# Kernel optimization log

Hardware: AMD Instinct MI355X
Metric: run time of the kernel (lower is better)

The kernel has to match this reference:

```python
import jax, jax.numpy as jnp
import numpy as np

SR = 48000
SECONDS = 2.0
T = int(SECONDS * SR)  # 96000 samples


def _shift(x, n):
    """Delay 1-D signal x by n samples, zero-filling (n may be a traced int >= 0)."""
    t = jnp.arange(x.shape[0])
    return jnp.where(t >= n, jnp.roll(x, n), jnp.zeros((), x.dtype))


def setup_inputs() -> dict:
    key = jax.random.key(0)
    k1, k2 = jax.random.split(key)
    excitation = jax.random.normal(k1, (T,), dtype=jnp.float32)
    pluckPosition = jax.random.uniform(k2, (1,), dtype=jnp.float32, minval=0.1, maxval=0.9)
    return {
        "length": 240,  # delay-line length in samples -> f0 = SR/length = 200 Hz
        "pluckPosition": pluckPosition,
        "excitation": excitation,
        "nut_gain": jnp.asarray(-0.99, jnp.float32),    # GuitarNuts reflection
        "bridge_gain": jnp.asarray(-0.995, jnp.float32),  # GuitarBridge reflection
        "bridge_b": jnp.asarray(0.5, jnp.float32),      # bridge one-zero lowpass coeff
        "disp_a": jnp.asarray(0.3, jnp.float32),        # dispersion FIR coeff
    }


def reference(length, pluckPosition, excitation, nut_gain, bridge_gain, bridge_b, disp_a):
    L = int(length)
    pluck = pluckPosition[0]
    nUp = jnp.round(L * pluck).astype(jnp.int32)   # StringSegment(nUp)
    nDown = jnp.int32(L) - nUp                      # StringSegment(nDown)

    def bridge_lp(x):
        # one-zero lowpass at the bridge: y[t] = (1-b)*x[t] + b*x[t-1]
        return (1.0 - bridge_b) * x + bridge_b * _shift(x, 1)

    def dispersion(x):
        # two-tap FIR dispersion filter: y[t] = a*x[t] + (1-a)*x[t-1]
        return disp_a * x + (1.0 - disp_a) * _shift(x, 1)

    def vibrate(l, r):
        # right-going wave: up segment -> dispersion -> down segment
        r2 = _shift(dispersion(_shift(r, nUp)), nDown)
        # left-going wave: down segment -> dispersion -> up segment
        l2 = _shift(dispersion(_shift(l, nDown)), nUp)
        return l2, r2

    # _start: inject excitation (split between the two traveling waves at pluck point)
    left0 = _shift(0.5 * excitation, nDown)
    right0 = _shift(0.5 * excitation, nUp)

    n_iter = T // L  # len(excitation) // int(length)

    def step(carry, _):
        l, r, acc = carry
        r_new = nut_gain * l                      # _lterminate: nut reflection of left wave
        l_new = bridge_gain * bridge_lp(r)        # _rterminate: bridge reflection of right wave
        l_new, r_new = vibrate(l_new, r_new)      # _vibrate: propagate through segments
        return (l_new, r_new, acc + l_new + r_new), None

    acc0 = left0 + right0
    (_, _, acc), _ = jax.lax.scan(step, (left0, right0, acc0), None, length=n_iter)
    return acc  # sum(left_signal) + sum(right_signal), shape [T]
```

## Files before the change

### kernel.cpp

```cpp
#include <hip/hip_runtime.h>


#define PREP_BLK 1024
#define SPAN_MAX 4640
#define SEQ_BLK  256

template<int NA, int NB>
static __device__ __forceinline__ void convT(const float* a, const float* b, float* c) {
#pragma unroll
    for (int i = 0; i < NA + NB - 1; ++i) c[i] = 0.f;
#pragma unroll
    for (int i = 0; i < NA; ++i)
#pragma unroll
        for (int j = 0; j < NB; ++j) c[i + j] += a[i] * b[j];
}

struct Base {
    int L, nUp, nDown;
    float gb, gn, g;
    float c0, c1, c2, d0, d1;
    float e[4];
};

static __device__ __forceinline__ Base mkbase(const int* Lp, const float* pk,
        const float* gnp, const float* gbp, const float* bbp, const float* dap) {
    Base b;
    b.L = Lp[0];
    b.gn = gnp[0]; b.gb = gbp[0];
    const float bb = bbp[0], da = dap[0];
    b.nUp   = (int)rintf((float)b.L * pk[0]);
    b.nDown = b.L - b.nUp;
    b.c0 = da * (1.f - bb);
    b.c1 = da * bb + (1.f - da) * (1.f - bb);
    b.c2 = (1.f - da) * bb;
    b.d0 = da; b.d1 = 1.f - da;
    b.e[0] = b.c0*b.d0;
    b.e[1] = b.c0*b.d1 + b.c1*b.d0;
    b.e[2] = b.c1*b.d1 + b.c2*b.d0;
    b.e[3] = b.c2*b.d1;
    b.g = b.gb * b.gn;
    return b;
}

__global__ __launch_bounds__(PREP_BLK, 1)
void prep_kernel(const int* Lp, const float* pk, const float* __restrict__ exc,
                 const float* gnp, const float* gbp, const float* bbp, const float* dap,
                 float* __restrict__ D4l, float* __restrict__ D4r, int T) {
    __shared__ float Dls[SPAN_MAX];
    __shared__ float Drs[SPAN_MAX];

    const Base B = mkbase(Lp, pk, gnp, gbp, bbp, dap);
    float p2[7], p3[10], p4[13], p5[16], p6[19], p7[22];
    convT<4,4>(B.e, B.e, p2);
    convT<7,4>(p2, B.e, p3);
    convT<7,7>(p2, p2, p4);
    convT<13,4>(p4, B.e, p5);
    convT<13,7>(p4, p2, p6);
    convT<13,10>(p4, p3, p7);
    const float g = B.g, g2 = g*g, g3 = g2*g, g4 = g2*g2, g5 = g4*g, g6 = g4*g2, g7 = g4*g3;

    const int P0   = 2 * B.L;
    const int H    = 7 * P0 + 21;
    const int span = PREP_BLK + H;
    const int t0   = blockIdx.x * PREP_BLK;
    const int base = t0 - H;

    const int mx = (B.nUp > B.nDown) ? B.nUp : B.nDown;
    const bool safe = (base - B.L - mx - 2) >= 0;

    for (int j = threadIdx.x; j < span; j += PREP_BLK) {
        const int s = base + j;
        float dl, dr;
        if (safe) {
            dl = 0.5f * exc[s - B.nDown]
               + (0.5f * B.gb) * (B.c0 * exc[s - B.L     - B.nUp]
                                + B.c1 * exc[s - B.L - 1 - B.nUp]
                                + B.c2 * exc[s - B.L - 2 - B.nUp]);
            dr = 0.5f * exc[s - B.nUp]
               + (0.5f * B.gn) * (B.d0 * exc[s - B.L     - B.nDown]
                                + B.d1 * exc[s - B.L - 1 - B.nDown]);
        } else {
            auto ex = [&](int i) -> float { return (i >= 0) ? exc[i] : 0.f; };
            if (s < 0) { dl = 0.f; dr = 0.f; }
            else {
                dl = 0.5f * ex(s - B.nDown)
                   + (0.5f * B.gb) * (B.c0 * ex(s - B.L     - B.nUp)
                                    + B.c1 * ex(s - B.L - 1 - B.nUp)
                                    + B.c2 * ex(s - B.L - 2 - B.nUp));
                dr = 0.5f * ex(s - B.nUp)
                   + (0.5f * B.gn) * (B.d0 * ex(s - B.L     - B.nDown)
                                    + B.d1 * ex(s - B.L - 1 - B.nDown));
            }
        }
        Dls[j] = dl; Drs[j] = dr;
    }
    __syncthreads();

    const int t = t0 + threadIdx.x;
    if (t < T) {
        const int p = H + threadIdx.x;
        float al = Dls[p], ar = Drs[p];
#pragma unroll
        for (int k = 0; k < 4;  ++k) { const int j = p -     P0 - k; const float w = g  * B.e[k]; al += w*Dls[j]; ar += w*Drs[j]; }
#pragma unroll
        for (int k = 0; k < 7;  ++k) { const int j = p - 2 * P0 - k; const float w = g2 * p2[k];  al += w*Dls[j]; ar += w*Drs[j]; }
#pragma unroll
        for (int k = 0; k < 10; ++k) { const int j = p - 3 * P0 - k; const float w = g3 * p3[k];  al += w*Dls[j]; ar += w*Drs[j]; }
#pragma unroll
        for (int k = 0; k < 13; ++k) { const int j = p - 4 * P0 - k; const float w = g4 * p4[k];  al += w*Dls[j]; ar += w*Drs[j]; }
#pragma unroll
        for (int k = 0; k < 16; ++k) { const int j = p - 5 * P0 - k; const float w = g5 * p5[k];  al += w*Dls[j]; ar += w*Drs[j]; }
#pragma unroll
        for (int k = 0; k < 19; ++k) { const int j = p - 6 * P0 - k; const float w = g6 * p6[k];  al += w*Dls[j]; ar += w*Drs[j]; }
#pragma unroll
        for (int k = 0; k < 22; ++k) { const int j = p - 7 * P0 - k; const float w = g7 * p7[k];  al += w*Dls[j]; ar += w*Drs[j]; }
        D4l[t] = al; D4r[t] = ar;
    }
}

__global__ __launch_bounds__(SEQ_BLK, 1)
void seq_kernel(const int* Lp, const float* pk, const float* gnp, const float* gbp,
                const float* bbp, const float* dap,
                float* __restrict__ Slw, float* __restrict__ Srw, int T) {
    __shared__ float4 pl[2][4][256];
    __shared__ float4 pre[4][6];

    const Base B = mkbase(Lp, pk, gnp, gbp, bbp, dap);
    float p2[7], p4[13], f[25];
    convT<4,4>(B.e, B.e, p2);
    convT<7,7>(p2, p2, p4);
    convT<13,13>(p4, p4, f);
    const float g2 = B.g * B.g, g4 = g2 * g2, G = g4 * g4;

    const int L = B.L, P = 16 * L, NA = L;
    const int lam = threadIdx.x;
    const bool act = lam < NA;
    float* __restrict__ DD = blockIdx.x ? Srw : Slw;

    {   float4* z = &pl[0][0][0];
        for (int i = lam; i < 2*4*256; i += SEQ_BLK) z[i] = float4{0,0,0,0};
        if (lam < 24) (&pre[0][0])[lam] = float4{0,0,0,0};
    }
    __syncthreads();

    const int nphase = (T + P - 1) / P;

    auto load16 = [&](int t, float4& a, float4& b, float4& c, float4& d) {
        if (t + 16 <= T) {
            a = *(const float4*)(DD + t);      b = *(const float4*)(DD + t + 4);
            c = *(const float4*)(DD + t + 8); d = *(const float4*)(DD + t + 12);
        } else {
            float tmp[16];
#pragma unroll
            for (int s = 0; s < 16; ++s) tmp[s] = (t + s < T) ? DD[t + s] : 0.f;
            a = float4{tmp[0],tmp[1],tmp[2],tmp[3]};   b = float4{tmp[4],tmp[5],tmp[6],tmp[7]};
            c = float4{tmp[8],tmp[9],tmp[10],tmp[11]}; d = float4{tmp[12],tmp[13],tmp[14],tmp[15]};
        }
    };

    float4 dE[4] = {{0,0,0,0},{0,0,0,0},{0,0,0,0},{0,0,0,0}};
    float4 dO[4] = {{0,0,0,0},{0,0,0,0},{0,0,0,0},{0,0,0,0}};
    if (act)               load16(lam << 4,     dE[0], dE[1], dE[2], dE[3]);
    if (act && nphase > 1) load16(P + (lam<<4), dO[0], dO[1], dO[2], dO[3]);

    float4 pS0{0,0,0,0}, pS1{0,0,0,0}, pS2{0,0,0,0}, pS3{0,0,0,0};

    auto do_phase = [&](int q, float4 (&dv)[4]) {
        const int par = q & 1, pp = par ^ 1, rs = (q + 2) & 3, wsl = q & 3;

        float4 B2{0,0,0,0}, B3{0,0,0,0}, A0{0,0,0,0}, A1{0,0,0,0}, A2{0,0,0,0}, A3{0,0,0,0};
        if (act) {
            if (lam >= 2) {
                B2 = pl[pp][2][lam-2]; B3 = pl[pp][3][lam-2];
                A0 = pl[pp][0][lam-1]; A1 = pl[pp][1][lam-1];
                A2 = pl[pp][2][lam-1]; A3 = pl[pp][3][lam-1];
            } else if (lam == 1) {
                B2 = pre[rs][4]; B3 = pre[rs][5];
                A0 = pl[pp][0][0]; A1 = pl[pp][1][0];
                A2 = pl[pp][2][0]; A3 = pl[pp][3][0];
            } else {
                B2 = pre[rs][0]; B3 = pre[rs][1];
                A0 = pre[rs][2]; A1 = pre[rs][3];
                A2 = pre[rs][4]; A3 = pre[rs][5];
            }
        }

        float S[16];
        if (act) {
            float cw[40];
            cw[0]=B2.x; cw[1]=B2.y; cw[2]=B2.z; cw[3]=B2.w;
            cw[4]=B3.x; cw[5]=B3.y; cw[6]=B3.z; cw[7]=B3.w;
            cw[8]=A0.x; cw[9]=A0.y; cw[10]=A0.z; cw[11]=A0.w;
            cw[12]=A1.x; cw[13]=A1.y; cw[14]=A1.z; cw[15]=A1.w;
            cw[16]=A2.x; cw[17]=A2.y; cw[18]=A2.z; cw[19]=A2.w;
            cw[20]=A3.x; cw[21]=A3.y; cw[22]=A3.z; cw[23]=A3.w;
            cw[24]=pS0.x; cw[25]=pS0.y; cw[26]=pS0.z; cw[27]=pS0.w;
            cw[28]=pS1.x; cw[29]=pS1.y; cw[30]=pS1.z; cw[31]=pS1.w;
            cw[32]=pS2.x; cw[33]=pS2.y; cw[34]=pS2.z; cw[35]=pS2.w;
            cw[36]=pS3.x; cw[37]=pS3.y; cw[38]=pS3.z; cw[39]=pS3.w;
            const float dvf[16] = {dv[0].x,dv[0].y,dv[0].z,dv[0].w,
                                   dv[1].x,dv[1].y,dv[1].z,dv[1].w,
                                   dv[2].x,dv[2].y,dv[2].z,dv[2].w,
                                   dv[3].x,dv[3].y,dv[3].z,dv[3].w};
#pragma unroll
            for (int s = 0; s < 16; ++s) {
                float a0 = 0.f, a1 = 0.f;
#pragma unroll
                for (int k = 0; k < 25; k += 2) a0 += f[k] * cw[24 + s - k];
#pragma unroll
                for (int k = 1; k < 25; k += 2) a1 += f[k] * cw[24 + s - k];
                S[s] = dvf[s] + G * (a0 + a1);
            }
        }

        if (act && (q + 2) < nphase) load16((q + 2) * P + (lam << 4), dv[0], dv[1], dv[2], dv[3]);

        if (act) {
            pS0 = float4{S[0],S[1],S[2],S[3]};   pS1 = float4{S[4],S[5],S[6],S[7]};
            pS2 = float4{S[8],S[9],S[10],S[11]}; pS3 = float4{S[12],S[13],S[14],S[15]};
            pl[par][0][lam] = pS0; pl[par][1][lam] = pS1;
            pl[par][2][lam] = pS2; pl[par][3][lam] = pS3;
            if (lam == NA - 2) { pre[wsl][0] = pS2; pre[wsl][1] = pS3; }
            if (lam == NA - 1) { pre[wsl][2] = pS0; pre[wsl][3] = pS1;
                                 pre[wsl][4] = pS2; pre[wsl][5] = pS3; }
            const int tg = q * P + (lam << 4);
            if (tg + 16 <= T) {
                *(float4*)(DD + tg)      = pS0; *(float4*)(DD + tg + 4)  = pS1;
                *(float4*)(DD + tg + 8)  = pS2; *(float4*)(DD + tg + 12) = pS3;
            } else {
#pragma unroll
                for (int s = 0; s < 16; ++s) if (tg + s < T) DD[tg + s] = S[s];
            }
        }

        asm volatile("s_waitcnt lgkmcnt(0)" ::: "memory");
        __builtin_amdgcn_sched_barrier(0);
        __builtin_amdgcn_s_barrier();
        __builtin_amdgcn_sched_barrier(0);
    };

    int q = 0;
    for (; q + 1 < nphase; q += 2) { do_phase(q, dE); do_phase(q + 1, dO); }
    if (q < nphase) do_phase(q, dE);
}

__global__ void add_kernel(const float* __restrict__ a, const float* __restrict__ b,
                           float* __restrict__ o, int T) {
    const int i = (blockIdx.x * blockDim.x + threadIdx.x) * 4;
    if (i + 4 <= T) {
        const float4 x = *(const float4*)(a + i);
        const float4 y = *(const float4*)(b + i);
        *(float4*)(o + i) = float4{x.x + y.x, x.y + y.y, x.z + y.z, x.w + y.w};
    } else if (i < T) {
        for (int s = i; s < T; ++s) o[s] = a[s] + b[s];
    }
}

extern "C" void kernel_launch(void* const* d_in, const int* in_sizes, int n_in,
                              void* d_out, int out_size, void* d_ws, size_t ws_size,
                              hipStream_t stream) {
    const int*   Lp  = (const int*)  d_in[0];
    const float* pk  = (const float*)d_in[1];
    const float* exc = (const float*)d_in[2];
    const float* gn  = (const float*)d_in[3];
    const float* gb  = (const float*)d_in[4];
    const float* bb  = (const float*)d_in[5];
    const float* da  = (const float*)d_in[6];
    float* out = (float*)d_out;
    float* D4l = (float*)d_ws;
    float* D4r = D4l + out_size;
    const int T = out_size;

    prep_kernel<<<(T + PREP_BLK - 1) / PREP_BLK, PREP_BLK, 0, stream>>>(
        Lp, pk, exc, gn, gb, bb, da, D4l, D4r, T);
    seq_kernel<<<2, SEQ_BLK, 0, stream>>>(Lp, pk, gn, gb, bb, da, D4l, D4r, T);
    add_kernel<<<(T / 4 + 255) / 256, 256, 0, stream>>>(D4l, D4r, out, T);
}
```

Measured before the change: 55.80 us.

## Halve per-thread span in sequential recurrence kernel and add clock warm-up probe

The sequential recurrence kernel now uses 2L threads, each computing 8 samples instead of 16, so per-thread FIR work per phase is halved. The shared-memory halo exchange is reworked to take three neighbour lanes and three carried-over boundary entries. A dummy FMA-spinning kernel is launched before the sequential kernel, apparently to raise GPU clocks. That probe adds launch time and extra work, and the larger block adds barrier cost across more waves.

Measured after the change: 56.18 us. No clear change (+0.7%).

```diff
diff --git a/kernel.cpp b/kernel.cpp
--- a/kernel.cpp
+++ b/kernel.cpp
@@ -3,7 +3,7 @@
 
 #define PREP_BLK 1024
 #define SPAN_MAX 4640
-#define SEQ_BLK  256
+#define SEQ_BLK  512
 
 template<int NA, int NB>
 static __device__ __forceinline__ void convT(const float* a, const float* b, float* c) {
@@ -118,11 +118,30 @@
     }
 }
 
+__global__ __launch_bounds__(256, 4)
+void clock_probe_kernel(int iters) {
+    float a0 = threadIdx.x * 1e-9f + 0.10f, a1 = a0 + 0.01f, a2 = a0 + 0.02f,
+          a3 = a0 + 0.03f, a4 = a0 + 0.04f, a5 = a0 + 0.05f, a6 = a0 + 0.06f,
+          a7 = a0 + 0.07f;
+    for (int i = 0; i < iters; ++i) {
+        a0 = __builtin_fmaf(a0, 0.9999f, 1e-7f);
+        a1 = __builtin_fmaf(a1, 0.9999f, 1e-7f);
+        a2 = __builtin_fmaf(a2, 0.9999f, 1e-7f);
+        a3 = __builtin_fmaf(a3, 0.9999f, 1e-7f);
+        a4 = __builtin_fmaf(a4, 0.9999f, 1e-7f);
+        a5 = __builtin_fmaf(a5, 0.9999f, 1e-7f);
+        a6 = __builtin_fmaf(a6, 0.9999f, 1e-7f);
+        a7 = __builtin_fmaf(a7, 0.9999f, 1e-7f);
+    }
+    asm volatile("" :: "v"(a0), "v"(a1), "v"(a2), "v"(a3),
+                       "v"(a4), "v"(a5), "v"(a6), "v"(a7));
+}
+
 __global__ __launch_bounds__(SEQ_BLK, 1)
 void seq_kernel(const int* Lp, const float* pk, const float* gnp, const float* gbp,
                 const float* bbp, const float* dap,
                 float* __restrict__ Slw, float* __restrict__ Srw, int T) {
-    __shared__ float4 pl[2][4][256];
+    __shared__ float4 pl[2][2][512];
     __shared__ float4 pre[4][6];
 
     const Base B = mkbase(Lp, pk, gnp, gbp, bbp, dap);
@@ -132,78 +151,73 @@
     convT<13,13>(p4, p4, f);
     const float g2 = B.g * B.g, g4 = g2 * g2, G = g4 * g4;
 
-    const int L = B.L, P = 16 * L, NA = L;
+    const int L = B.L, P = 16 * L, NA = 2 * L;
     const int lam = threadIdx.x;
     const bool act = lam < NA;
     float* __restrict__ DD = blockIdx.x ? Srw : Slw;
 
     {   float4* z = &pl[0][0][0];
-        for (int i = lam; i < 2*4*256; i += SEQ_BLK) z[i] = float4{0,0,0,0};
+        for (int i = lam; i < 2*2*512; i += SEQ_BLK) z[i] = float4{0,0,0,0};
         if (lam < 24) (&pre[0][0])[lam] = float4{0,0,0,0};
     }
     __syncthreads();
 
     const int nphase = (T + P - 1) / P;
 
-    auto load16 = [&](int t, float4& a, float4& b, float4& c, float4& d) {
-        if (t + 16 <= T) {
-            a = *(const float4*)(DD + t);      b = *(const float4*)(DD + t + 4);
-            c = *(const float4*)(DD + t + 8); d = *(const float4*)(DD + t + 12);
+    auto load8 = [&](int t, float4& a, float4& b) {
+        if (t + 8 <= T) {
+            a = *(const float4*)(DD + t); b = *(const float4*)(DD + t + 4);
         } else {
-            float tmp[16];
-#pragma unroll
-            for (int s = 0; s < 16; ++s) tmp[s] = (t + s < T) ? DD[t + s] : 0.f;
-            a = float4{tmp[0],tmp[1],tmp[2],tmp[3]};   b = float4{tmp[4],tmp[5],tmp[6],tmp[7]};
-            c = float4{tmp[8],tmp[9],tmp[10],tmp[11]}; d = float4{tmp[12],tmp[13],tmp[14],tmp[15]};
+            float tmp[8];
+#pragma unroll
+            for (int s = 0; s < 8; ++s) tmp[s] = (t + s < T) ? DD[t + s] : 0.f;
+            a = float4{tmp[0],tmp[1],tmp[2],tmp[3]};
+            b = float4{tmp[4],tmp[5],tmp[6],tmp[7]};
         }
     };
 
-    float4 dE[4] = {{0,0,0,0},{0,0,0,0},{0,0,0,0},{0,0,0,0}};
-    float4 dO[4] = {{0,0,0,0},{0,0,0,0},{0,0,0,0},{0,0,0,0}};
-    if (act)               load16(lam << 4,     dE[0], dE[1], dE[2], dE[3]);
-    if (act && nphase > 1) load16(P + (lam<<4), dO[0], dO[1], dO[2], dO[3]);
-
-    float4 pS0{0,0,0,0}, pS1{0,0,0,0}, pS2{0,0,0,0}, pS3{0,0,0,0};
-
-    auto do_phase = [&](int q, float4 (&dv)[4]) {
+    float4 dE[2] = {{0,0,0,0},{0,0,0,0}};
+    float4 dO[2] = {{0,0,0,0},{0,0,0,0}};
+    if (act)               load8(lam << 3,       dE[0], dE[1]);
+    if (act && nphase > 1) load8(P + (lam << 3), dO[0], dO[1]);
+
+    float4 pS0{0,0,0,0}, pS1{0,0,0,0};
+
+    auto do_phase = [&](int q, float4 (&dv)[2]) {
         const int par = q & 1, pp = par ^ 1, rs = (q + 2) & 3, wsl = q & 3;
 
-        float4 B2{0,0,0,0}, B3{0,0,0,0}, A0{0,0,0,0}, A1{0,0,0,0}, A2{0,0,0,0}, A3{0,0,0,0};
+        float4 W0{0,0,0,0}, W1{0,0,0,0}, W2{0,0,0,0},
+               W3{0,0,0,0}, W4{0,0,0,0}, W5{0,0,0,0};
         if (act) {
-            if (lam >= 2) {
-                B2 = pl[pp][2][lam-2]; B3 = pl[pp][3][lam-2];
-                A0 = pl[pp][0][lam-1]; A1 = pl[pp][1][lam-1];
-                A2 = pl[pp][2][lam-1]; A3 = pl[pp][3][lam-1];
+            if (lam >= 3) {
+                W0 = pl[pp][0][lam-3]; W1 = pl[pp][1][lam-3];
+                W2 = pl[pp][0][lam-2]; W3 = pl[pp][1][lam-2];
+                W4 = pl[pp][0][lam-1]; W5 = pl[pp][1][lam-1];
+            } else if (lam == 2) {
+                W0 = pre[rs][4]; W1 = pre[rs][5];
+                W2 = pl[pp][0][0]; W3 = pl[pp][1][0];
+                W4 = pl[pp][0][1]; W5 = pl[pp][1][1];
             } else if (lam == 1) {
-                B2 = pre[rs][4]; B3 = pre[rs][5];
-                A0 = pl[pp][0][0]; A1 = pl[pp][1][0];
-                A2 = pl[pp][2][0]; A3 = pl[pp][3][0];
+                W0 = pre[rs][2]; W1 = pre[rs][3];
+                W2 = pre[rs][4]; W3 = pre[rs][5];
+                W4 = pl[pp][0][0]; W5 = pl[pp][1][0];
             } else {
-                B2 = pre[rs][0]; B3 = pre[rs][1];
-                A0 = pre[rs][2]; A1 = pre[rs][3];
-                A2 = pre[rs][4]; A3 = pre[rs][5];
-            }
-        }
-
-        float S[16];
+                W0 = pre[rs][0]; W1 = pre[rs][1];
+                W2 = pre[rs][2]; W3 = pre[rs][3];
+                W4 = pre[rs][4]; W5 = pre[rs][5];
+            }
+        }
+
+        float S[8];
         if (act) {
-            float cw[40];
-            cw[0]=B2.x; cw[1]=B2.y; cw[2]=B2.z; cw[3]=B2.w;
-            cw[4]=B3.x; cw[5]=B3.y; cw[6]=B3.z; cw[7]=B3.w;
-            cw[8]=A0.x; cw[9]=A0.y; cw[10]=A0.z; cw[11]=A0.w;
-            cw[12]=A1.x; cw[13]=A1.y; cw[14]=A1.z; cw[15]=A1.w;
-            cw[16]=A2.x; cw[17]=A2.y; cw[18]=A2.z; cw[19]=A2.w;
-            cw[20]=A3.x; cw[21]=A3.y; cw[22]=A3.z; cw[23]=A3.w;
-            cw[24]=pS0.x; cw[25]=pS0.y; cw[26]=pS0.z; cw[27]=pS0.w;
-            cw[28]=pS1.x; cw[29]=pS1.y; cw[30]=pS1.z; cw[31]=pS1.w;
-            cw[32]=pS2.x; cw[33]=pS2.y; cw[34]=pS2.z; cw[35]=pS2.w;
-            cw[36]=pS3.x; cw[37]=pS3.y; cw[38]=pS3.z; cw[39]=pS3.w;
-            const float dvf[16] = {dv[0].x,dv[0].y,dv[0].z,dv[0].w,
-                                   dv[1].x,dv[1].y,dv[1].z,dv[1].w,
-                                   dv[2].x,dv[2].y,dv[2].z,dv[2].w,
-                                   dv[3].x,dv[3].y,dv[3].z,dv[3].w};
-#pragma unroll
-            for (int s = 0; s < 16; ++s) {
+            const float cw[32] = {W0.x,W0.y,W0.z,W0.w, W1.x,W1.y,W1.z,W1.w,
+                                  W2.x,W2.y,W2.z,W2.w, W3.x,W3.y,W3.z,W3.w,
+                                  W4.x,W4.y,W4.z,W4.w, W5.x,W5.y,W5.z,W5.w,
+                                  pS0.x,pS0.y,pS0.z,pS0.w, pS1.x,pS1.y,pS1.z,pS1.w};
+            const float dvf[8] = {dv[0].x,dv[0].y,dv[0].z,dv[0].w,
+                                  dv[1].x,dv[1].y,dv[1].z,dv[1].w};
+#pragma unroll
+            for (int s = 0; s < 8; ++s) {
                 float a0 = 0.f, a1 = 0.f;
 #pragma unroll
                 for (int k = 0; k < 25; k += 2) a0 += f[k] * cw[24 + s - k];
@@ -211,25 +225,25 @@
                 for (int k = 1; k < 25; k += 2) a1 += f[k] * cw[24 + s - k];
                 S[s] = dvf[s] + G * (a0 + a1);
             }
-        }
-
-        if (act && (q + 2) < nphase) load16((q + 2) * P + (lam << 4), dv[0], dv[1], dv[2], dv[3]);
+            pS0 = float4{S[0],S[1],S[2],S[3]};
+            pS1 = float4{S[4],S[5],S[6],S[7]};
+
+            pl[par][0][lam] = pS0; pl[par][1][lam] = pS1;
+            if (lam == NA - 3) { pre[wsl][0] = pS0; pre[wsl][1] = pS1; }
+            if (lam == NA - 2) { pre[wsl][2] = pS0; pre[wsl][3] = pS1; }
+            if (lam == NA - 1) { pre[wsl][4] = pS0; pre[wsl][5] = pS1; }
+        }
+
+        if (act && (q + 2) < nphase) load8((q + 2) * P + (lam << 3), dv[0], dv[1]);
 
         if (act) {
-            pS0 = float4{S[0],S[1],S[2],S[3]};   pS1 = float4{S[4],S[5],S[6],S[7]};
-            pS2 = float4{S[8],S[9],S[10],S[11]}; pS3 = float4{S[12],S[13],S[14],S[15]};
-            pl[par][0][lam] = pS0; pl[par][1][lam] = pS1;
-            pl[par][2][lam] = pS2; pl[par][3][lam] = pS3;
-            if (lam == NA - 2) { pre[wsl][0] = pS2; pre[wsl][1] = pS3; }
-            if (lam == NA - 1) { pre[wsl][2] = pS0; pre[wsl][3] = pS1;
-                                 pre[wsl][4] = pS2; pre[wsl][5] = pS3; }
-            const int tg = q * P + (lam << 4);
-            if (tg + 16 <= T) {
-                *(float4*)(DD + tg)      = pS0; *(float4*)(DD + tg + 4)  = pS1;
-                *(float4*)(DD + tg + 8)  = pS2; *(float4*)(DD + tg + 12) = pS3;
+            const int tg = q * P + (lam << 3);
+            if (tg + 8 <= T) {
+                *(float4*)(DD + tg)     = pS0;
+                *(float4*)(DD + tg + 4) = pS1;
             } else {
 #pragma unroll
-                for (int s = 0; s < 16; ++s) if (tg + s < T) DD[tg + s] = S[s];
+                for (int s = 0; s < 8; ++s) if (tg + s < T) DD[tg + s] = S[s];
             }
         }
 
@@ -273,6 +287,7 @@
 
     prep_kernel<<<(T + PREP_BLK - 1) / PREP_BLK, PREP_BLK, 0, stream>>>(
         Lp, pk, exc, gn, gb, bb, da, D4l, D4r, T);
+    clock_probe_kernel<<<1024, 256, 0, stream>>>(64);
     seq_kernel<<<2, SEQ_BLK, 0, stream>>>(Lp, pk, gn, gb, bb, da, D4l, D4r, T);
     add_kernel<<<(T / 4 + 255) / 256, 256, 0, stream>>>(D4l, D4r, out, T);
 }
```
